# Kernel optimization log

Hardware: AMD Instinct MI355X
Metric: run time of the kernel (lower is better)

## Reference

```python
import jax, jax.numpy as jnp
import numpy as np
from jax import lax

B, D, H, STEPS = 16384, 256, 256, 25


def setup_inputs() -> dict:
    key = jax.random.key(0)
    k1, k2, k3, k4 = jax.random.split(key, 4)
    s1 = 1.0 / np.sqrt(D)
    s2 = 1.0 / np.sqrt(H)
    return {
        "z0": jax.random.normal(k1, (B, D), dtype=jnp.float32),
        "t_range": jnp.linspace(0.0, 1.0, STEPS, dtype=jnp.float32),
        "W1": jax.random.normal(k2, (D, H), dtype=jnp.float32) * s1,
        "b1": jnp.zeros((H,), dtype=jnp.float32),
        "wt": jax.random.normal(k3, (H,), dtype=jnp.float32) * 0.1,
        "W2": jax.random.normal(k4, (H, D), dtype=jnp.float32) * s2,
        "b2": jnp.zeros((D,), dtype=jnp.float32),
    }


def reference(z0, t_range, W1, b1, wt, W2, b2):
    # Euler solver: zt <- zt + dt * f(zt, t) for every t in t_range
    # (matches euler_solver: note it steps at ALL 25 grid points, incl. t_end)
    dt = t_range[1] - t_range[0]

    def dynamics(z, t):
        h = jnp.tanh(z @ W1 + b1 + t * wt)  # [B, H]
        return h @ W2 + b2                   # [B, D]

    def step(z, t):
        return z + dt * dynamics(z, t), None

    zT, _ = lax.scan(step, z0, t_range)
    return zT
```

## Files before the change

kernel.cpp:

```cpp
#include <hip/hip_runtime.h>

typedef short bf16x8 __attribute__((ext_vector_type(8)));
typedef float f32x4  __attribute__((ext_vector_type(4)));

#define NSTEP 25
#define SROW  264
#define LDSB  (32 * SROW)

__device__ __forceinline__ unsigned short f2bf(float x) {
    union { float f; unsigned int u; } v; v.f = x;
    unsigned int r = v.u + 0x7FFFu + ((v.u >> 16) & 1u);
    return (unsigned short)(r >> 16);
}

#if __has_builtin(__builtin_amdgcn_cvt_pk_bf16_f32)
typedef __bf16 bfv2 __attribute__((ext_vector_type(2)));
__device__ __forceinline__ unsigned int pk2bf(float a, float b) {
    union { bfv2 v; unsigned int u; } c;
    c.v = __builtin_amdgcn_cvt_pk_bf16_f32(a, b);
    return c.u;
}
#else
__device__ __forceinline__ unsigned int pk2bf(float a, float b) {
    return (unsigned int)f2bf(a) | ((unsigned int)f2bf(b) << 16);
}
#endif

#if __has_builtin(__builtin_amdgcn_exp2f)
#define EXP2F __builtin_amdgcn_exp2f
#else
#define EXP2F exp2f
#endif

#define C2LOG2E 2.8853900817779268f

__device__ __forceinline__ float tanh_pre(float y, float btc) {
    float e = EXP2F(fmaf(y, C2LOG2E, btc));
    return 1.0f - 2.0f * __builtin_amdgcn_rcpf(e + 1.0f);
}

__global__ void prep_all(const float* __restrict__ W1,
                         const float* __restrict__ W2,
                         const float* __restrict__ b2,
                         const float* __restrict__ t_range,
                         unsigned short* __restrict__ Wr,
                         unsigned short* __restrict__ W21r,
                         float* __restrict__ c1)
{
    __shared__ float row[256];
    int b = blockIdx.x;
    if (b < 257) {
        int i = b, j = threadIdx.x;
        row[j] = (i < 256) ? W2[i * 256 + j] : b2[j];
        __syncthreads();
        float a0 = 0.f, a1 = 0.f, a2 = 0.f, a3 = 0.f;
#pragma unroll
        for (int d = 0; d < 256; d += 16) {
            float w[16];
#pragma unroll
            for (int u = 0; u < 16; ++u) w[u] = W1[(d + u) * 256 + j];
#pragma unroll
            for (int u = 0; u < 16; u += 4) {
                a0 = fmaf(row[d + u + 0], w[u + 0], a0);
                a1 = fmaf(row[d + u + 1], w[u + 1], a1);
                a2 = fmaf(row[d + u + 2], w[u + 2], a2);
                a3 = fmaf(row[d + u + 3], w[u + 3], a3);
            }
        }
        float acc = (a0 + a1) + (a2 + a3);
        if (i < 256) {
            float dt = t_range[1] - t_range[0];
            int p  = (i & ~31) | ((i & 15) << 1) | ((i >> 4) & 1);
            int kc = p >> 5, q = (p >> 3) & 3, jj = p & 7;
            W21r[kc * 8192 + j * 32 + q * 8 + jj] = f2bf(dt * acc);
        } else {
            c1[j] = acc;
        }
    } else {
        int bb = b - 257;
        const float* src = (bb < 256) ? W1 : W2;
        unsigned short* dst = Wr + ((bb < 256) ? 0 : 65536);
        int k = bb & 255;
        int n = threadIdx.x;
        int p  = (k & ~31) | ((k & 15) << 1) | ((k >> 4) & 1);
        int kc = p >> 5, q = (p >> 3) & 3, jj = p & 7;
        dst[kc * 8192 + n * 32 + q * 8 + jj] = f2bf(src[k * 256 + n]);
    }
}

#define STEP_BODY(BUF)                                                          \
  {                                                                             \
    const int buf = (BUF);                                                      \
    _Pragma("unroll")                                                           \
    for (int band = 0; band < 2; ++band)                                        \
      _Pragma("unroll")                                                         \
      for (int r = 0; r < 4; ++r) {                                             \
        int m = band * 16 + q * 4 + r;                                          \
        float h0 = tanh_pre(y[band][0][r], btc[0]);                             \
        float h1 = tanh_pre(y[band][1][r], btc[1]);                             \
        S[band][0][r] += h0; S[band][1][r] += h1;                               \
        *(unsigned int*)&As[buf + m * SROW + n0 + l15 * 2] = pk2bf(h0, h1);     \
      }                                                                         \
    btc[0] += dbtc[0]; btc[1] += dbtc[1];                                       \
    __syncthreads();                                                            \
    __builtin_amdgcn_s_setprio(1);                                              \
    _Pragma("unroll")                                                           \
    for (int kc = 0; kc < 8; ++kc) {                                            \
      bf16x8 a0 = *(const bf16x8*)&As[buf + l15 * SROW + kc * 32 + q * 8];      \
      bf16x8 a1 = *(const bf16x8*)&As[buf + (16 + l15) * SROW + kc * 32 + q * 8];\
      _Pragma("unroll")                                                         \
      for (int tt = 0; tt < 2; ++tt) {                                          \
        y[0][tt] = __builtin_amdgcn_mfma_f32_16x16x32_bf16(a0, w21f[kc][tt],    \
                                                           y[0][tt], 0, 0, 0); \
        y[1][tt] = __builtin_amdgcn_mfma_f32_16x16x32_bf16(a1, w21f[kc][tt],    \
                                                           y[1][tt], 0, 0, 0); \
      }                                                                         \
    }                                                                           \
    __builtin_amdgcn_s_setprio(0);                                              \
  }

__global__ __launch_bounds__(512, 4) void ode_main(
    const float* __restrict__ z0,
    const float* __restrict__ t_range,
    const float* __restrict__ b1,
    const float* __restrict__ wt,
    const float* __restrict__ b2,
    const unsigned short* __restrict__ W1r,
    const unsigned short* __restrict__ W2r,
    const unsigned short* __restrict__ W21r,
    const float* __restrict__ c1,
    float* __restrict__ out)
{
    __shared__ __align__(16) unsigned short As[2 * LDSB];

    const int tid  = threadIdx.x;
    const int wave = tid >> 6;
    const int lane = tid & 63;
    const int q    = lane >> 4;
    const int l15  = lane & 15;
    const int row0 = blockIdx.x * 32;
    const int n0   = wave * 32;

    const float dt = t_range[1] - t_range[0];

    float btc[2], dbtc[2];
#pragma unroll
    for (int tt = 0; tt < 2; ++tt) {
        int n = n0 + tt * 16 + l15;
        btc[tt]  = b1[n] * C2LOG2E;
        dbtc[tt] = dt * (wt[n] + c1[n]) * C2LOG2E;
    }

#pragma unroll
    for (int band = 0; band < 2; ++band)
#pragma unroll
        for (int r = 0; r < 4; ++r) {
            int m = band * 16 + q * 4 + r;
            const float* zr = &z0[(row0 + m) * 256 + n0];
            *(unsigned int*)&As[m * SROW + n0 + l15 * 2] =
                pk2bf(zr[l15], zr[16 + l15]);
        }
    __syncthreads();

    f32x4 y[2][2];
#pragma unroll
    for (int band = 0; band < 2; ++band)
#pragma unroll
        for (int tt = 0; tt < 2; ++tt) y[band][tt] = f32x4{0.f, 0.f, 0.f, 0.f};
#pragma unroll
    for (int kc = 0; kc < 8; ++kc) {
        bf16x8 a[2];
#pragma unroll
        for (int band = 0; band < 2; ++band)
            a[band] = *(const bf16x8*)&As[(band * 16 + l15) * SROW + kc * 32 + q * 8];
#pragma unroll
        for (int tt = 0; tt < 2; ++tt) {
            bf16x8 bb = *(const bf16x8*)&W1r[kc * 8192 + (n0 + tt * 16 + l15) * 32 + q * 8];
#pragma unroll
            for (int band = 0; band < 2; ++band)
                y[band][tt] = __builtin_amdgcn_mfma_f32_16x16x32_bf16(
                    a[band], bb, y[band][tt], 0, 0, 0);
        }
    }

    bf16x8 w21f[8][2];
#pragma unroll
    for (int kc = 0; kc < 8; ++kc)
#pragma unroll
        for (int tt = 0; tt < 2; ++tt)
            w21f[kc][tt] = *(const bf16x8*)&W21r[kc * 8192 + (n0 + tt * 16 + l15) * 32 + q * 8];

    f32x4 S[2][2];
#pragma unroll
    for (int band = 0; band < 2; ++band)
#pragma unroll
        for (int tt = 0; tt < 2; ++tt) S[band][tt] = f32x4{0.f, 0.f, 0.f, 0.f};

    if ((blockIdx.x >> 8) & 1) __builtin_amdgcn_s_sleep(22);

#pragma unroll 1
    for (int it = 0; it < (NSTEP - 1) / 2; ++it) {
        STEP_BODY(LDSB)
        STEP_BODY(0)
    }

#pragma unroll
    for (int band = 0; band < 2; ++band)
#pragma unroll
        for (int r = 0; r < 4; ++r)
#pragma unroll
            for (int tt = 0; tt < 2; ++tt)
                S[band][tt][r] += tanh_pre(y[band][tt][r], btc[tt]);

    {
        const int buf = LDSB;
#pragma unroll
        for (int band = 0; band < 2; ++band)
#pragma unroll
            for (int r = 0; r < 4; ++r) {
                int m = band * 16 + q * 4 + r;
                *(unsigned int*)&As[buf + m * SROW + n0 + l15 * 2] =
                    pk2bf(S[band][0][r], S[band][1][r]);
            }
        __syncthreads();

        f32x4 acc[2][2];
#pragma unroll
        for (int band = 0; band < 2; ++band)
#pragma unroll
            for (int tt = 0; tt < 2; ++tt) acc[band][tt] = f32x4{0.f, 0.f, 0.f, 0.f};
#pragma unroll
        for (int kc = 0; kc < 8; ++kc) {
            bf16x8 a[2];
#pragma unroll
            for (int band = 0; band < 2; ++band)
                a[band] = *(const bf16x8*)&As[buf + (band * 16 + l15) * SROW + kc * 32 + q * 8];
#pragma unroll
            for (int tt = 0; tt < 2; ++tt) {
                bf16x8 bb = *(const bf16x8*)&W2r[kc * 8192 + (n0 + tt * 16 + l15) * 32 + q * 8];
#pragma unroll
                for (int band = 0; band < 2; ++band)
                    acc[band][tt] = __builtin_amdgcn_mfma_f32_16x16x32_bf16(
                        a[band], bb, acc[band][tt], 0, 0, 0);
            }
        }

        const float cb2 = (float)NSTEP * dt;
#pragma unroll
        for (int band = 0; band < 2; ++band)
#pragma unroll
            for (int tt = 0; tt < 2; ++tt) {
                float b2v = b2[n0 + tt * 16 + l15];
#pragma unroll
                for (int r = 0; r < 4; ++r) {
                    int idx = (row0 + band * 16 + q * 4 + r) * 256 + n0 + tt * 16 + l15;
                    out[idx] = z0[idx] + dt * acc[band][tt][r] + cb2 * b2v;
                }
            }
    }
}

extern "C" void kernel_launch(void* const* d_in, const int* in_sizes, int n_in,
                              void* d_out, int out_size, void* d_ws, size_t ws_size,
                              hipStream_t stream) {
    const float* z0      = (const float*)d_in[0];
    const float* t_range = (const float*)d_in[1];
    const float* W1      = (const float*)d_in[2];
    const float* b1      = (const float*)d_in[3];
    const float* wt      = (const float*)d_in[4];
    const float* W2      = (const float*)d_in[5];
    const float* b2      = (const float*)d_in[6];

    unsigned short* Wr = (unsigned short*)d_ws;
    unsigned short* W1r  = Wr;
    unsigned short* W2r  = Wr + 65536;
    unsigned short* W21r = Wr + 131072;
    float*          c1   = (float*)(Wr + 196608);

    prep_all<<<769, 256, 0, stream>>>(W1, W2, b2, t_range, Wr, W21r, c1);
    ode_main<<<512, 512, 0, stream>>>(z0, t_range, b1, wt, b2,
                                      W1r, W2r, W21r, c1, (float*)d_out);
}
```

Before: 152.2 us.

## Interleave two row tiles per block to overlap MFMA with tanh epilogue

Each block now processes 64 rows as two 32-row tiles. The step loop alternates so that one tile's MFMA chain runs while the other tile's tanh, accumulation and LDS stores run, aiming to hide the dependency latency between the matmul and the nonlinearity. The grid is halved to 256 blocks, launch bounds drop to 2 waves per EU, the setprio and sleep staggering are removed, and register pressure roughly doubles for accumulators. The loop runs 24 iterations of paired regions, which matches the original 24 steps per tile plus a final epilogue.

Measured after the change: 149.6 us. No clear change (-1.7%).

```diff
diff --git a/kernel.cpp b/kernel.cpp
--- a/kernel.cpp
+++ b/kernel.cpp
@@ -88,38 +88,35 @@
     }
 }
 
-#define STEP_BODY(BUF)                                                          \
+#define REGION(YM, RBASE, YS, SS, SBASE, BTCS)                                  \
   {                                                                             \
-    const int buf = (BUF);                                                      \
+    _Pragma("unroll")                                                           \
+    for (int kc = 0; kc < 8; ++kc) {                                            \
+      bf16x8 a0 = *(const bf16x8*)&As[(RBASE) + l15 * SROW + kc * 32 + q * 8];  \
+      bf16x8 a1 = *(const bf16x8*)&As[(RBASE) + (16 + l15) * SROW + kc * 32 + q * 8]; \
+      _Pragma("unroll")                                                         \
+      for (int tt = 0; tt < 2; ++tt) {                                          \
+        YM[0][tt] = __builtin_amdgcn_mfma_f32_16x16x32_bf16(a0, w21f[kc][tt],   \
+                                                            YM[0][tt], 0, 0, 0);\
+        YM[1][tt] = __builtin_amdgcn_mfma_f32_16x16x32_bf16(a1, w21f[kc][tt],   \
+                                                            YM[1][tt], 0, 0, 0);\
+      }                                                                         \
+    }                                                                           \
     _Pragma("unroll")                                                           \
     for (int band = 0; band < 2; ++band)                                        \
       _Pragma("unroll")                                                         \
       for (int r = 0; r < 4; ++r) {                                             \
         int m = band * 16 + q * 4 + r;                                          \
-        float h0 = tanh_pre(y[band][0][r], btc[0]);                             \
-        float h1 = tanh_pre(y[band][1][r], btc[1]);                             \
-        S[band][0][r] += h0; S[band][1][r] += h1;                               \
-        *(unsigned int*)&As[buf + m * SROW + n0 + l15 * 2] = pk2bf(h0, h1);     \
+        float h0 = tanh_pre(YS[band][0][r], BTCS[0]);                           \
+        float h1 = tanh_pre(YS[band][1][r], BTCS[1]);                           \
+        SS[band][0][r] += h0; SS[band][1][r] += h1;                             \
+        *(unsigned int*)&As[(SBASE) + m * SROW + n0 + l15 * 2] = pk2bf(h0, h1); \
       }                                                                         \
-    btc[0] += dbtc[0]; btc[1] += dbtc[1];                                       \
+    BTCS[0] += dbtc[0]; BTCS[1] += dbtc[1];                                     \
     __syncthreads();                                                            \
-    __builtin_amdgcn_s_setprio(1);                                              \
-    _Pragma("unroll")                                                           \
-    for (int kc = 0; kc < 8; ++kc) {                                            \
-      bf16x8 a0 = *(const bf16x8*)&As[buf + l15 * SROW + kc * 32 + q * 8];      \
-      bf16x8 a1 = *(const bf16x8*)&As[buf + (16 + l15) * SROW + kc * 32 + q * 8];\
-      _Pragma("unroll")                                                         \
-      for (int tt = 0; tt < 2; ++tt) {                                          \
-        y[0][tt] = __builtin_amdgcn_mfma_f32_16x16x32_bf16(a0, w21f[kc][tt],    \
-                                                           y[0][tt], 0, 0, 0); \
-        y[1][tt] = __builtin_amdgcn_mfma_f32_16x16x32_bf16(a1, w21f[kc][tt],    \
-                                                           y[1][tt], 0, 0, 0); \
-      }                                                                         \
-    }                                                                           \
-    __builtin_amdgcn_s_setprio(0);                                              \
   }
 
-__global__ __launch_bounds__(512, 4) void ode_main(
+__global__ __launch_bounds__(512, 2) void ode_main(
     const float* __restrict__ z0,
     const float* __restrict__ t_range,
     const float* __restrict__ b1,
@@ -134,114 +131,148 @@
     __shared__ __align__(16) unsigned short As[2 * LDSB];
 
     const int tid  = threadIdx.x;
-    const int wave = tid >> 6;
     const int lane = tid & 63;
     const int q    = lane >> 4;
     const int l15  = lane & 15;
-    const int row0 = blockIdx.x * 32;
-    const int n0   = wave * 32;
+    const int row0 = blockIdx.x * 64;
+    const int n0   = (tid >> 6) * 32;
 
     const float dt = t_range[1] - t_range[0];
 
-    float btc[2], dbtc[2];
+    float btcA[2], btcB[2], dbtc[2];
 #pragma unroll
     for (int tt = 0; tt < 2; ++tt) {
         int n = n0 + tt * 16 + l15;
-        btc[tt]  = b1[n] * C2LOG2E;
+        btcA[tt] = b1[n] * C2LOG2E;
+        btcB[tt] = btcA[tt];
         dbtc[tt] = dt * (wt[n] + c1[n]) * C2LOG2E;
     }
+
+#pragma unroll
+    for (int tile = 0; tile < 2; ++tile)
+#pragma unroll
+        for (int band = 0; band < 2; ++band)
+#pragma unroll
+            for (int r = 0; r < 4; ++r) {
+                int m = band * 16 + q * 4 + r;
+                const float* zr = &z0[(row0 + tile * 32 + m) * 256 + n0];
+                *(unsigned int*)&As[tile * LDSB + m * SROW + n0 + l15 * 2] =
+                    pk2bf(zr[l15], zr[16 + l15]);
+            }
+    __syncthreads();
+
+    f32x4 yA[2][2], yB[2][2];
+#pragma unroll
+    for (int band = 0; band < 2; ++band)
+#pragma unroll
+        for (int tt = 0; tt < 2; ++tt) {
+            yA[band][tt] = f32x4{0.f, 0.f, 0.f, 0.f};
+            yB[band][tt] = f32x4{0.f, 0.f, 0.f, 0.f};
+        }
+#pragma unroll
+    for (int kc = 0; kc < 8; ++kc) {
+        bf16x8 aA[2], aB[2];
+#pragma unroll
+        for (int band = 0; band < 2; ++band) {
+            aA[band] = *(const bf16x8*)&As[(band * 16 + l15) * SROW + kc * 32 + q * 8];
+            aB[band] = *(const bf16x8*)&As[LDSB + (band * 16 + l15) * SROW + kc * 32 + q * 8];
+        }
+#pragma unroll
+        for (int tt = 0; tt < 2; ++tt) {
+            bf16x8 bb = *(const bf16x8*)&W1r[kc * 8192 + (n0 + tt * 16 + l15) * 32 + q * 8];
+#pragma unroll
+            for (int band = 0; band < 2; ++band) {
+                yA[band][tt] = __builtin_amdgcn_mfma_f32_16x16x32_bf16(
+                    aA[band], bb, yA[band][tt], 0, 0, 0);
+                yB[band][tt] = __builtin_amdgcn_mfma_f32_16x16x32_bf16(
+                    aB[band], bb, yB[band][tt], 0, 0, 0);
+            }
+        }
+    }
+    __syncthreads();
+
+    bf16x8 w21f[8][2];
+#pragma unroll
+    for (int kc = 0; kc < 8; ++kc)
+#pragma unroll
+        for (int tt = 0; tt < 2; ++tt)
+            w21f[kc][tt] = *(const bf16x8*)&W21r[kc * 8192 + (n0 + tt * 16 + l15) * 32 + q * 8];
+
+    f32x4 SA[2][2], SB[2][2];
+#pragma unroll
+    for (int band = 0; band < 2; ++band)
+#pragma unroll
+        for (int tt = 0; tt < 2; ++tt) {
+            SA[band][tt] = f32x4{0.f, 0.f, 0.f, 0.f};
+            SB[band][tt] = f32x4{0.f, 0.f, 0.f, 0.f};
+        }
 
 #pragma unroll
     for (int band = 0; band < 2; ++band)
 #pragma unroll
         for (int r = 0; r < 4; ++r) {
             int m = band * 16 + q * 4 + r;
-            const float* zr = &z0[(row0 + m) * 256 + n0];
-            *(unsigned int*)&As[m * SROW + n0 + l15 * 2] =
-                pk2bf(zr[l15], zr[16 + l15]);
-        }
+            float h0 = tanh_pre(yA[band][0][r], btcA[0]);
+            float h1 = tanh_pre(yA[band][1][r], btcA[1]);
+            SA[band][0][r] += h0; SA[band][1][r] += h1;
+            *(unsigned int*)&As[m * SROW + n0 + l15 * 2] = pk2bf(h0, h1);
+        }
+    btcA[0] += dbtc[0]; btcA[1] += dbtc[1];
     __syncthreads();
 
-    f32x4 y[2][2];
+#pragma unroll 1
+    for (int j = 0; j < NSTEP - 1; ++j) {
+        REGION(yA, 0,    yB, SB, LDSB, btcB)
+        REGION(yB, LDSB, yA, SA, 0,    btcA)
+    }
+
 #pragma unroll
     for (int band = 0; band < 2; ++band)
 #pragma unroll
-        for (int tt = 0; tt < 2; ++tt) y[band][tt] = f32x4{0.f, 0.f, 0.f, 0.f};
-#pragma unroll
-    for (int kc = 0; kc < 8; ++kc) {
-        bf16x8 a[2];
-#pragma unroll
-        for (int band = 0; band < 2; ++band)
-            a[band] = *(const bf16x8*)&As[(band * 16 + l15) * SROW + kc * 32 + q * 8];
-#pragma unroll
-        for (int tt = 0; tt < 2; ++tt) {
-            bf16x8 bb = *(const bf16x8*)&W1r[kc * 8192 + (n0 + tt * 16 + l15) * 32 + q * 8];
-#pragma unroll
-            for (int band = 0; band < 2; ++band)
-                y[band][tt] = __builtin_amdgcn_mfma_f32_16x16x32_bf16(
-                    a[band], bb, y[band][tt], 0, 0, 0);
-        }
-    }
-
-    bf16x8 w21f[8][2];
-#pragma unroll
-    for (int kc = 0; kc < 8; ++kc)
-#pragma unroll
-        for (int tt = 0; tt < 2; ++tt)
-            w21f[kc][tt] = *(const bf16x8*)&W21r[kc * 8192 + (n0 + tt * 16 + l15) * 32 + q * 8];
-
-    f32x4 S[2][2];
-#pragma unroll
-    for (int band = 0; band < 2; ++band)
-#pragma unroll
-        for (int tt = 0; tt < 2; ++tt) S[band][tt] = f32x4{0.f, 0.f, 0.f, 0.f};
-
-    if ((blockIdx.x >> 8) & 1) __builtin_amdgcn_s_sleep(22);
-
-#pragma unroll 1
-    for (int it = 0; it < (NSTEP - 1) / 2; ++it) {
-        STEP_BODY(LDSB)
-        STEP_BODY(0)
-    }
-
-#pragma unroll
-    for (int band = 0; band < 2; ++band)
-#pragma unroll
         for (int r = 0; r < 4; ++r)
 #pragma unroll
             for (int tt = 0; tt < 2; ++tt)
-                S[band][tt][r] += tanh_pre(y[band][tt][r], btc[tt]);
+                SB[band][tt][r] += tanh_pre(yB[band][tt][r], btcB[tt]);
 
     {
-        const int buf = LDSB;
 #pragma unroll
         for (int band = 0; band < 2; ++band)
 #pragma unroll
             for (int r = 0; r < 4; ++r) {
                 int m = band * 16 + q * 4 + r;
-                *(unsigned int*)&As[buf + m * SROW + n0 + l15 * 2] =
-                    pk2bf(S[band][0][r], S[band][1][r]);
+                *(unsigned int*)&As[m * SROW + n0 + l15 * 2] =
+                    pk2bf(SA[band][0][r], SA[band][1][r]);
+                *(unsigned int*)&As[LDSB + m * SROW + n0 + l15 * 2] =
+                    pk2bf(SB[band][0][r], SB[band][1][r]);
             }
         __syncthreads();
 
-        f32x4 acc[2][2];
+        f32x4 accA[2][2], accB[2][2];
 #pragma unroll
         for (int band = 0; band < 2; ++band)
 #pragma unroll
-            for (int tt = 0; tt < 2; ++tt) acc[band][tt] = f32x4{0.f, 0.f, 0.f, 0.f};
+            for (int tt = 0; tt < 2; ++tt) {
+                accA[band][tt] = f32x4{0.f, 0.f, 0.f, 0.f};
+                accB[band][tt] = f32x4{0.f, 0.f, 0.f, 0.f};
+            }
 #pragma unroll
         for (int kc = 0; kc < 8; ++kc) {
-            bf16x8 a[2];
-#pragma unroll
-            for (int band = 0; band < 2; ++band)
-                a[band] = *(const bf16x8*)&As[buf + (band * 16 + l15) * SROW + kc * 32 + q * 8];
+            bf16x8 aA[2], aB[2];
+#pragma unroll
+            for (int band = 0; band < 2; ++band) {
+                aA[band] = *(const bf16x8*)&As[(band * 16 + l15) * SROW + kc * 32 + q * 8];
+                aB[band] = *(const bf16x8*)&As[LDSB + (band * 16 + l15) * SROW + kc * 32 + q * 8];
+            }
 #pragma unroll
             for (int tt = 0; tt < 2; ++tt) {
                 bf16x8 bb = *(const bf16x8*)&W2r[kc * 8192 + (n0 + tt * 16 + l15) * 32 + q * 8];
 #pragma unroll
-                for (int band = 0; band < 2; ++band)
-                    acc[band][tt] = __builtin_amdgcn_mfma_f32_16x16x32_bf16(
-                        a[band], bb, acc[band][tt], 0, 0, 0);
+                for (int band = 0; band < 2; ++band) {
+                    accA[band][tt] = __builtin_amdgcn_mfma_f32_16x16x32_bf16(
+                        aA[band], bb, accA[band][tt], 0, 0, 0);
+                    accB[band][tt] = __builtin_amdgcn_mfma_f32_16x16x32_bf16(
+                        aB[band], bb, accB[band][tt], 0, 0, 0);
+                }
             }
         }
 
@@ -253,8 +284,10 @@
                 float b2v = b2[n0 + tt * 16 + l15];
 #pragma unroll
                 for (int r = 0; r < 4; ++r) {
-                    int idx = (row0 + band * 16 + q * 4 + r) * 256 + n0 + tt * 16 + l15;
-                    out[idx] = z0[idx] + dt * acc[band][tt][r] + cb2 * b2v;
+                    int idxA = (row0 + band * 16 + q * 4 + r) * 256 + n0 + tt * 16 + l15;
+                    int idxB = idxA + 32 * 256;
+                    out[idxA] = z0[idxA] + dt * accA[band][tt][r] + cb2 * b2v;
+                    out[idxB] = z0[idxB] + dt * accB[band][tt][r] + cb2 * b2v;
                 }
             }
     }
@@ -278,6 +311,6 @@
     float*          c1   = (float*)(Wr + 196608);
 
     prep_all<<<769, 256, 0, stream>>>(W1, W2, b2, t_range, Wr, W21r, c1);
-    ode_main<<<512, 512, 0, stream>>>(z0, t_range, b1, wt, b2,
+    ode_main<<<256, 512, 0, stream>>>(z0, t_range, b1, wt, b2,
                                       W1r, W2r, W21r, c1, (float*)d_out);
 }
```
